# Kernel tuning notes

Measured on AMD Instinct MI355X. Metric: run time of the kernel, lower is better.

## Reference

```python
import jax, jax.numpy as jnp
import numpy as np


def setup_inputs() -> dict:
    key = jax.random.key(0)
    ks = jax.random.split(key, 7)
    b, c, h, w = 4, 256, 64, 64
    ci = c // 2
    inp = {
        "x0": jax.random.normal(ks[0], (b, 2 * c, h, w), dtype=jnp.float32),
        "x": jax.random.normal(ks[1], (b, c, h, w), dtype=jnp.float32),
        "x_dsm": jax.random.normal(ks[2], (b, c, h, w), dtype=jnp.float32),
        # 1x1 conv weights, stored as [out_ch, in_ch]
        "w_phi": jax.random.normal(ks[3], (ci, c), dtype=jnp.float32) * 0.02,
        "w_theta": jax.random.normal(ks[4], (ci, c), dtype=jnp.float32) * 0.02,
        "w_g": jax.random.normal(ks[5], (c, 2 * c), dtype=jnp.float32) * 0.02,
        "w_mask": jax.random.normal(ks[6], (2 * c, c), dtype=jnp.float32) * 0.02,
    }
    return inp


def reference(x0, x, x_dsm, w_phi, w_theta, w_g, w_mask):
    b, c, h, w = x.shape
    ci = c // 2
    n = h * w
    # 1x1 convs as channel matmuls
    phi = jnp.einsum('oc,bchw->bohw', w_phi, x).reshape(b, ci, n)            # [b, ci, N]
    theta = jnp.einsum('oc,bchw->bohw', w_theta, x_dsm).reshape(b, ci, n)    # [b, ci, N]
    theta = theta.transpose(0, 2, 1)                                         # [b, N, ci]
    g = jnp.einsum('oc,bchw->bohw', w_g, x0).reshape(b, c, n).transpose(0, 2, 1)  # [b, N, c]
    scores = jnp.matmul(theta, phi)                                          # [b, N, N]
    # NOTE: original uses nn.Softmax(dim=1) -> normalize over the FIRST N axis
    attn = jax.nn.softmax(scores, axis=1)
    out = jnp.matmul(attn, g)                                                # [b, N, c]
    out = out.transpose(0, 2, 1).reshape(b, c, h, w)
    mask = jnp.einsum('oc,bchw->bohw', w_mask, out)                          # [b, 2c, h, w]
    return mask + x0
```

## Files before the change

### kernel.cpp

```cpp
#include <hip/hip_runtime.h>
#include <math.h>

#define NB 4
#define NC 256
#define NCI 128
#define NC2 512
#define NPOS 4096
#define ISPLIT 8

using bf16x8 = __attribute__((ext_vector_type(8))) short;
using f32x4  = __attribute__((ext_vector_type(4))) float;
using f32x16 = __attribute__((ext_vector_type(16))) float;

__device__ inline unsigned short f2bf(float f) {
  unsigned int u = __float_as_uint(f);
  u = (u + 0x7fffu + ((u >> 16) & 1u)) >> 16;
  return (unsigned short)u;
}
__device__ inline float bf2f(short s) {
  return __uint_as_float(((unsigned int)(unsigned short)s) << 16);
}

__global__ void k_cast4(const float* __restrict__ s0, short* __restrict__ d0, int n0,
                        const float* __restrict__ s1, short* __restrict__ d1, int n1,
                        const float* __restrict__ s2, short* __restrict__ d2, int n2,
                        const float* __restrict__ s3, short* __restrict__ d3, int n3) {
  int i = blockIdx.x * 256 + threadIdx.x;
  if (i < n0) { d0[i] = (short)f2bf(s0[i]); return; } i -= n0;
  if (i < n1) { d1[i] = (short)f2bf(s1[i]); return; } i -= n1;
  if (i < n2) { d2[i] = (short)f2bf(s2[i]); return; } i -= n2;
  if (i < n3) { d3[i] = (short)f2bf(s3[i]); }
}

__global__ __launch_bounds__(256) void k_tcast_all(
    const float* __restrict__ x, const float* __restrict__ xdsm,
    const float* __restrict__ x0, short* __restrict__ xT,
    short* __restrict__ xdT, short* __restrict__ x0T) {
  __shared__ float t[64][65];
  const int tid = threadIdx.x;
  const int y = blockIdx.y, c0 = blockIdx.x * 64, b = blockIdx.z;
  const float* in; short* out; int R, r0;
  if (y < 4)      { in = x;    out = xT;  R = NC;  r0 = y * 64; }
  else if (y < 8) { in = xdsm; out = xdT; R = NC;  r0 = (y - 4) * 64; }
  else            { in = x0;   out = x0T; R = NC2; r0 = (y - 8) * 64; }
  const size_t inBs = (size_t)R * NPOS, outBs = (size_t)NPOS * R;
  {
    int r = tid >> 2, cc = (tid & 3) * 16;
    const float* ib = in + (size_t)b * inBs + (size_t)(r0 + r) * NPOS + c0 + cc;
#pragma unroll
    for (int i = 0; i < 4; ++i) {
      float4 v = *(const float4*)(ib + i * 4);
      t[r][cc + i * 4 + 0] = v.x; t[r][cc + i * 4 + 1] = v.y;
      t[r][cc + i * 4 + 2] = v.z; t[r][cc + i * 4 + 3] = v.w;
    }
  }
  __syncthreads();
  {
    int c = tid >> 2, rr = (tid & 3) * 16;
    __align__(16) short v[16];
#pragma unroll
    for (int i = 0; i < 16; ++i) v[i] = (short)f2bf(t[rr + i][c]);
    short* ob = out + (size_t)b * outBs + (size_t)(c0 + c) * R + r0 + rr;
    *(int4*)(ob) = *(const int4*)(v);
    *(int4*)(ob + 8) = *(const int4*)(v + 8);
  }
}

__global__ __launch_bounds__(256) void k_tcast4(
    const short* __restrict__ inP, short* __restrict__ out) {
  __shared__ float t[64][65];
  const int tid = threadIdx.x;
  const int r0 = blockIdx.y * 64, c0 = blockIdx.x * 64, b = blockIdx.z;
  {
    int r = tid >> 2, cc = (tid & 3) * 16;
    float tacc[16] = {};
#pragma unroll
    for (int p = 0; p < 4; ++p) {
      const short* ib = inP + ((size_t)p * NB + b) * NC * NPOS +
                        (size_t)(r0 + r) * NPOS + c0 + cc;
      bf16x8 a = *(const bf16x8*)(ib);
      bf16x8 a2 = *(const bf16x8*)(ib + 8);
#pragma unroll
      for (int i = 0; i < 8; ++i) { tacc[i] += bf2f(a[i]); tacc[8 + i] += bf2f(a2[i]); }
    }
#pragma unroll
    for (int i = 0; i < 16; ++i) t[r][cc + i] = tacc[i];
  }
  __syncthreads();
  {
    int c = tid >> 2, rr = (tid & 3) * 16;
    __align__(16) short v[16];
#pragma unroll
    for (int i = 0; i < 16; ++i) v[i] = (short)f2bf(t[rr + i][c]);
    short* ob = out + (size_t)b * (size_t)NPOS * NC + (size_t)(c0 + c) * NC + r0 + rr;
    *(int4*)(ob) = *(const int4*)(v);
    *(int4*)(ob + 8) = *(const int4*)(v + 8);
  }
}

template<bool OUT_BF16, bool HAS_RES>
__global__ __launch_bounds__(256, 2) void k_gemm(
    const short* __restrict__ A, const short* __restrict__ B,
    void* __restrict__ outv, const float* __restrict__ res,
    int K, int sN, size_t aBs, size_t bBs, size_t oBs) {
  __shared__ short As[2][64 * 64];
  __shared__ short Bs_[2][64 * 64];
  const int tid = threadIdx.x, lane = tid & 63, w = tid >> 6;
  const int x = lane & 15, q = lane >> 4;
  const int wm = (w & 1) * 32, wn = (w >> 1) * 32;
  const int n0 = blockIdx.x * 64, m0 = blockIdx.y * 64, b = blockIdx.z;
  const short* Ab = A + (size_t)b * aBs + (size_t)m0 * K;
  const short* Bb = B + (size_t)b * bBs + (size_t)n0 * K;
  const int r = tid >> 2, cth = tid & 3;
  f32x4 acc[2][2];
  acc[0][0] = acc[0][1] = acc[1][0] = acc[1][1] = (f32x4){0.f, 0.f, 0.f, 0.f};
  int4 ra[2], rb[2];
  const int NK = K >> 6;
#define GLOAD(kt)                                                              \
  { _Pragma("unroll") for (int i = 0; i < 2; ++i) {                            \
      ra[i] = *(const int4*)(Ab + (size_t)r * K + (kt) * 64 + (cth + i * 4) * 8); \
      rb[i] = *(const int4*)(Bb + (size_t)r * K + (kt) * 64 + (cth + i * 4) * 8); } }
#define GWRITE(buf)                                                            \
  { _Pragma("unroll") for (int i = 0; i < 2; ++i) {                            \
      *(int4*)(&As[buf][r * 64 + (((cth + i * 4) ^ (r & 7)) * 8)]) = ra[i];    \
      *(int4*)(&Bs_[buf][r * 64 + (((cth + i * 4) ^ (r & 7)) * 8)]) = rb[i]; } }
  GLOAD(0); GWRITE(0); __syncthreads();
  int cur = 0;
  for (int kt = 0; kt < NK; ++kt) {
    if (kt + 1 < NK) GLOAD(kt + 1);
    bf16x8 af[2][2], bfr[2][2];
#pragma unroll
    for (int ms = 0; ms < 2; ++ms) {
      int rowm = wm + ms * 16 + x;
#pragma unroll
      for (int ks = 0; ks < 2; ++ks)
        af[ms][ks] = *(const bf16x8*)(&As[cur][rowm * 64 + (((ks * 4 + q) ^ (rowm & 7)) * 8)]);
    }
#pragma unroll
    for (int ns = 0; ns < 2; ++ns) {
      int rown = wn + ns * 16 + x;
#pragma unroll
      for (int ks = 0; ks < 2; ++ks)
        bfr[ns][ks] = *(const bf16x8*)(&Bs_[cur][rown * 64 + (((ks * 4 + q) ^ (rown & 7)) * 8)]);
    }
#pragma unroll
    for (int ms = 0; ms < 2; ++ms)
#pragma unroll
      for (int ns = 0; ns < 2; ++ns)
#pragma unroll
        for (int ks = 0; ks < 2; ++ks)
          acc[ms][ns] = __builtin_amdgcn_mfma_f32_16x16x32_bf16(
              af[ms][ks], bfr[ns][ks], acc[ms][ns], 0, 0, 0);
    if (kt + 1 < NK) GWRITE(cur ^ 1);
    __syncthreads();
    cur ^= 1;
  }
#pragma unroll
  for (int ms = 0; ms < 2; ++ms)
#pragma unroll
    for (int ns = 0; ns < 2; ++ns) {
      int n = n0 + wn + ns * 16 + x;
      int m = m0 + wm + ms * 16 + q * 4;
      size_t off = (size_t)b * oBs + (size_t)n * sN + m;
      if (OUT_BF16) {
        __align__(8) short pv[4];
#pragma unroll
        for (int j = 0; j < 4; ++j) pv[j] = (short)f2bf(acc[ms][ns][j]);
        *(uint2*)((short*)outv + off) = *(const uint2*)pv;
      } else {
        float4 v = {acc[ms][ns][0], acc[ms][ns][1], acc[ms][ns][2], acc[ms][ns][3]};
        if (HAS_RES) {
          float4 rv = *(const float4*)(res + off);
          v.x += rv.x; v.y += rv.y; v.z += rv.z; v.w += rv.w;
        }
        *(float4*)((float*)outv + off) = v;
      }
    }
#undef GLOAD
#undef GWRITE
}

__global__ __launch_bounds__(256, 4) void k_lsum(
    const short* __restrict__ phiB, const short* __restrict__ thetaB,
    float* __restrict__ plsum) {
  __shared__ short thT[2][64 * 128];
  const int tid = threadIdx.x, lane = tid & 63, w = tid >> 6;
  const int x = lane & 15, q = lane >> 4;
  const int j0 = blockIdx.x * 64, iy = blockIdx.y, b = blockIdx.z;
  const short* phb = phiB + (size_t)b * NPOS * NCI;
  const short* thb = thetaB + (size_t)b * NPOS * NCI + (size_t)iy * (NPOS / ISPLIT) * NCI;
  bf16x8 af[4];
  {
    const short* pr = phb + (size_t)(j0 + w * 16 + x) * NCI;
#pragma unroll
    for (int kk = 0; kk < 4; ++kk) af[kk] = *(const bf16x8*)(pr + kk * 32 + q * 8);
  }
  float lsum[4] = {0.f, 0.f, 0.f, 0.f};
  int4 rt[4];
  const int NIT = NPOS / ISPLIT / 64;
#define LSUM_LOAD(it)                                                         \
  { _Pragma("unroll") for (int r = 0; r < 4; ++r) {                           \
      int s = tid + r * 256; int row = s >> 4, c = s & 15;                    \
      rt[r] = *(const int4*)(thb + (size_t)((it) * 64 + row) * NCI + c * 8); } }
#define LSUM_WRITE(buf)                                                       \
  { _Pragma("unroll") for (int r = 0; r < 4; ++r) {                           \
      int s = tid + r * 256; int row = s >> 4, c = s & 15;                    \
      *(int4*)(&thT[buf][row * 128 + ((c ^ (row & 7)) * 8)]) = rt[r]; } }
  LSUM_LOAD(0); LSUM_WRITE(0); __syncthreads();
  int cur = 0;
  for (int it = 0; it < NIT; ++it) {
    if (it + 1 < NIT) LSUM_LOAD(it + 1);
#pragma unroll
    for (int ii = 0; ii < 4; ++ii) {
      f32x4 s = {0.f, 0.f, 0.f, 0.f};
      int row = ii * 16 + x;
      int sw = row & 7;
#pragma unroll
      for (int kk = 0; kk < 4; ++kk) {
        bf16x8 bfv = *(const bf16x8*)(&thT[cur][row * 128 + (((kk * 4 + q) ^ sw) * 8)]);
        s = __builtin_amdgcn_mfma_f32_16x16x32_bf16(af[kk], bfv, s, 0, 0, 0);
      }
#pragma unroll
      for (int r = 0; r < 4; ++r) lsum[r] += __expf(s[r]);
    }
    if (it + 1 < NIT) LSUM_WRITE(cur ^ 1);
    __syncthreads();
    cur ^= 1;
  }
#pragma unroll
  for (int m = 1; m < 16; m <<= 1)
#pragma unroll
    for (int r = 0; r < 4; ++r) lsum[r] += __shfl_xor(lsum[r], m);
  if (x == 0) {
#pragma unroll
    for (int r = 0; r < 4; ++r)
      plsum[((size_t)(b * ISPLIT + iy) << 12) + j0 + w * 16 + 4 * q + r] = lsum[r];
  }
#undef LSUM_LOAD
#undef LSUM_WRITE
}

__global__ void k_lcomb(const float* __restrict__ plsum, float* __restrict__ linv) {
  int i = blockIdx.x * 256 + threadIdx.x;
  int b = i >> 12, j = i & (NPOS - 1);
  float s = 0.f;
#pragma unroll
  for (int t = 0; t < ISPLIT; ++t) s += plsum[((size_t)(b * ISPLIT + t) << 12) + j];
  linv[i] = 1.0f / s;
}

__global__ void k_scale_g(short* __restrict__ gB, const float* __restrict__ linv) {
  size_t e = ((size_t)blockIdx.x * 256 + threadIdx.x) * 8;
  int b = (int)(e >> 20);
  int p = (int)(e & (NPOS - 1));
  __align__(16) short v[8];
  *(int4*)v = *(const int4*)(gB + e);
  const float* lv = linv + ((size_t)b << 12) + p;
#pragma unroll
  for (int k = 0; k < 8; ++k) v[k] = (short)f2bf(bf2f(v[k]) * lv[k]);
  *(int4*)(gB + e) = *(const int4*)v;
}

__global__ __launch_bounds__(256, 2) void k_attn(
    const short* __restrict__ phiB, const short* __restrict__ thetaB,
    const short* __restrict__ gB, short* __restrict__ omidP) {
  __shared__ short phiT[2][32 * 128];
  __shared__ short gT[2][256 * 32];
  __shared__ short pT[4][32 * 32];
  const int tid = threadIdx.x, lane = tid & 63, w = tid >> 6;
  const int il = lane & 31, h = lane >> 5;
  const int key = (il >> 1) & 3;
  const int i0 = blockIdx.x * 128, jq = blockIdx.y, b = blockIdx.z;
  const short* phb = phiB + (size_t)b * NPOS * NCI;
  const short* thb = thetaB + (size_t)b * NPOS * NCI;
  const short* gb = gB + (size_t)b * NC * NPOS;
  short* om = omidP + ((size_t)(jq * NB + b)) * NC * NPOS;

  bf16x8 tf[8];
  {
    const short* tr = thb + (size_t)(i0 + w * 32 + il) * NCI;
#pragma unroll
    for (int kk = 0; kk < 8; ++kk) tf[kk] = *(const bf16x8*)(tr + kk * 16 + h * 8);
  }
  f32x16 acc[8];
#pragma unroll
  for (int i = 0; i < 8; ++i)
#pragma unroll
    for (int r = 0; r < 16; ++r) acc[i][r] = 0.f;

  int4 rphi[2], rg[4];
  const int NT = 32;
  const int jbase = jq * 32;
#define ATTN_LOAD(jt)                                                          \
  { _Pragma("unroll") for (int r = 0; r < 2; ++r) {                            \
      int s = tid + r * 256; int row = s >> 4, c = s & 15;                     \
      rphi[r] = *(const int4*)(phb + (size_t)((jbase + (jt)) * 32 + row) * NCI + c * 8); } \
    _Pragma("unroll") for (int r = 0; r < 4; ++r) {                            \
      int s = tid + r * 256; int cc = s >> 2, c4 = s & 3;                      \
      rg[r] = *(const int4*)(gb + (size_t)cc * NPOS + (jbase + (jt)) * 32 + c4 * 8); } }
#define ATTN_WRITE(buf)                                                        \
  { _Pragma("unroll") for (int r = 0; r < 2; ++r) {                            \
      int s = tid + r * 256; int row = s >> 4, c = s & 15;                     \
      *(int4*)(&phiT[buf][row * 128 + ((c ^ (row & 7)) * 8)]) = rphi[r]; }     \
    _Pragma("unroll") for (int r = 0; r < 4; ++r) {                            \
      int s = tid + r * 256; int cc = s >> 2, c4 = s & 3;                      \
      *(int4*)(&gT[buf][cc * 32 + ((c4 ^ ((cc >> 1) & 3)) * 8)]) = rg[r]; } }
  ATTN_LOAD(0); ATTN_WRITE(0); __syncthreads();
  int cur = 0;
  for (int jt = 0; jt < NT; ++jt) {
    if (jt + 1 < NT) ATTN_LOAD(jt + 1);
    {
      const short* PH = &phiT[cur][0];
      short* PW = &pT[w][0];
      f32x16 s16;
#pragma unroll
      for (int r = 0; r < 16; ++r) s16[r] = 0.f;
      const int swp = il & 7;
#pragma unroll
      for (int kk = 0; kk < 8; ++kk) {
        bf16x8 a = *(const bf16x8*)(PH + il * 128 + (((2 * kk + h) ^ swp) * 8));
        s16 = __builtin_amdgcn_mfma_f32_32x32x16_bf16(a, tf[kk], s16, 0, 0, 0);
      }
#pragma unroll
      for (int g2 = 0; g2 < 4; ++g2) {
        unsigned short p0 = f2bf(__expf(s16[4 * g2 + 0]));
        unsigned short p1 = f2bf(__expf(s16[4 * g2 + 1]));
        unsigned short p2 = f2bf(__expf(s16[4 * g2 + 2]));
        unsigned short p3 = f2bf(__expf(s16[4 * g2 + 3]));
        unsigned int lo = (unsigned int)p0 | ((unsigned int)p1 << 16);
        unsigned int hi2 = (unsigned int)p2 | ((unsigned int)p3 << 16);
        *(uint2*)(PW + il * 32 + ((g2 ^ key) * 8) + 4 * h) = make_uint2(lo, hi2);
      }
      const short* GT = &gT[cur][0];
      bf16x8 pa[2];
#pragma unroll
      for (int jh2 = 0; jh2 < 2; ++jh2)
        pa[jh2] = *(const bf16x8*)(PW + il * 32 + (((2 * jh2 + h) ^ key) * 8));
#pragma unroll
      for (int ct = 0; ct < 8; ++ct) {
#pragma unroll
        for (int jh2 = 0; jh2 < 2; ++jh2) {
          bf16x8 bg = *(const bf16x8*)(GT + (ct * 32 + il) * 32 + (((2 * jh2 + h) ^ key) * 8));
          acc[ct] = __builtin_amdgcn_mfma_f32_32x32x16_bf16(pa[jh2], bg, acc[ct], 0, 0, 0);
        }
      }
    }
    if (jt + 1 < NT) ATTN_WRITE(cur ^ 1);
    __syncthreads();
    cur ^= 1;
  }
#pragma unroll
  for (int ct = 0; ct < 8; ++ct)
#pragma unroll
    for (int g2 = 0; g2 < 4; ++g2) {
      __align__(8) short pv[4];
#pragma unroll
      for (int e = 0; e < 4; ++e) pv[e] = (short)f2bf(acc[ct][4 * g2 + e]);
      size_t o = (size_t)(ct * 32 + il) * NPOS + i0 + w * 32 + 8 * g2 + 4 * h;
      *(uint2*)(om + o) = *(const uint2*)pv;
    }
#undef ATTN_LOAD
#undef ATTN_WRITE
}

extern "C" void kernel_launch(void* const* d_in, const int* in_sizes, int n_in,
                              void* d_out, int out_size, void* d_ws, size_t ws_size,
                              hipStream_t stream) {
  (void)in_sizes; (void)n_in; (void)out_size; (void)ws_size;
  const float* x0      = (const float*)d_in[0];
  const float* x       = (const float*)d_in[1];
  const float* x_dsm   = (const float*)d_in[2];
  const float* w_phi   = (const float*)d_in[3];
  const float* w_theta = (const float*)d_in[4];
  const float* w_g     = (const float*)d_in[5];
  const float* w_mask  = (const float*)d_in[6];
  float* outp = (float*)d_out;

  short* sp = (short*)d_ws;
  short* wb_phi   = sp; sp += 32768;
  short* wb_theta = sp; sp += 32768;
  short* wb_g     = sp; sp += 131072;
  short* wb_mask  = sp; sp += 131072;
  short* xT   = sp; sp += (size_t)NB * NPOS * NC;
  short* xdT  = sp; sp += (size_t)NB * NPOS * NC;
  short* x0T  = sp; sp += (size_t)NB * NPOS * NC2;
  short* phiB   = sp; sp += (size_t)NB * NPOS * NCI;
  short* thetaB = sp; sp += (size_t)NB * NPOS * NCI;
  short* gBuf   = sp; sp += (size_t)NB * NC * NPOS;
  float* linv = (float*)sp; sp += 2 * (size_t)NB * NPOS;
  float* plsum = (float*)sp;
  short* omidP = xT;
  short* omidT = phiB;

  k_cast4<<<dim3(1280), 256, 0, stream>>>(w_phi, wb_phi, 32768,
                                          w_theta, wb_theta, 32768,
                                          w_g, wb_g, 131072,
                                          w_mask, wb_mask, 131072);

  k_tcast_all<<<dim3(64, 16, NB), 256, 0, stream>>>(x, x_dsm, x0, xT, xdT, x0T);

  k_gemm<true, false><<<dim3(64, 2, NB), 256, 0, stream>>>(
      wb_phi, xT, phiB, nullptr, NC, NCI, 0, (size_t)NPOS * NC, (size_t)NPOS * NCI);
  k_gemm<true, false><<<dim3(64, 2, NB), 256, 0, stream>>>(
      wb_theta, xdT, thetaB, nullptr, NC, NCI, 0, (size_t)NPOS * NC, (size_t)NPOS * NCI);
  k_gemm<true, false><<<dim3(4, 64, NB), 256, 0, stream>>>(
      x0T, wb_g, gBuf, nullptr, NC2, NPOS, (size_t)NPOS * NC2, 0, (size_t)NC * NPOS);

  k_lsum<<<dim3(NPOS / 64, ISPLIT, NB), 256, 0, stream>>>(phiB, thetaB, plsum);
  k_lcomb<<<dim3(NB * NPOS / 256), 256, 0, stream>>>(plsum, linv);
  k_scale_g<<<dim3(2048), 256, 0, stream>>>(gBuf, linv);

  k_attn<<<dim3(NPOS / 128, 4, NB), 256, 0, stream>>>(phiB, thetaB, gBuf, omidP);

  k_tcast4<<<dim3(64, 4, NB), 256, 0, stream>>>(omidP, omidT);

  k_gemm<false, true><<<dim3(8, 64, NB), 256, 0, stream>>>(
      omidT, wb_mask, outp, x0, NC, NPOS, (size_t)NPOS * NC, 0, (size_t)NC2 * NPOS);
}
```

Measured before the change: 236.9 us.

## Rewrite column-sum kernel with 32x32x16 MFMA and 128-column blocks

The softmax denominator kernel now computes each tile with 32x32x16 bf16 MFMAs, so every wave covers 32 phi columns instead of 16 and each block covers 128 columns. The theta tile per iteration shrinks to 32 rows, and theta is placed in the A operand so the 16 accumulator values per lane all belong to one output column. That lets the per-lane exp sums be combined with a single cross-half shuffle instead of a 16-lane butterfly. The intent is to halve the grid and the redundant theta LDS traffic per column and to reduce per-tile overhead. In exchange it needs more registers for the phi fragments and runs twice as many, shorter loop iterations, with more barriers.

```diff
diff --git a/kernel.cpp b/kernel.cpp
--- a/kernel.cpp
+++ b/kernel.cpp
@@ -183,59 +183,51 @@
 __global__ __launch_bounds__(256, 4) void k_lsum(
     const short* __restrict__ phiB, const short* __restrict__ thetaB,
     float* __restrict__ plsum) {
-  __shared__ short thT[2][64 * 128];
+  __shared__ short thT[2][32 * 128];
   const int tid = threadIdx.x, lane = tid & 63, w = tid >> 6;
-  const int x = lane & 15, q = lane >> 4;
-  const int j0 = blockIdx.x * 64, iy = blockIdx.y, b = blockIdx.z;
+  const int il = lane & 31, h = lane >> 5;
+  const int j0 = blockIdx.x * 128, iy = blockIdx.y, b = blockIdx.z;
   const short* phb = phiB + (size_t)b * NPOS * NCI;
   const short* thb = thetaB + (size_t)b * NPOS * NCI + (size_t)iy * (NPOS / ISPLIT) * NCI;
-  bf16x8 af[4];
-  {
-    const short* pr = phb + (size_t)(j0 + w * 16 + x) * NCI;
-#pragma unroll
-    for (int kk = 0; kk < 4; ++kk) af[kk] = *(const bf16x8*)(pr + kk * 32 + q * 8);
-  }
-  float lsum[4] = {0.f, 0.f, 0.f, 0.f};
-  int4 rt[4];
-  const int NIT = NPOS / ISPLIT / 64;
+  bf16x8 pf[8];
+  {
+    const short* pr = phb + (size_t)(j0 + w * 32 + il) * NCI;
+#pragma unroll
+    for (int kk = 0; kk < 8; ++kk) pf[kk] = *(const bf16x8*)(pr + kk * 16 + h * 8);
+  }
+  float lsum = 0.f;
+  int4 rt[2];
+  const int NIT = NPOS / ISPLIT / 32;
 #define LSUM_LOAD(it)                                                         \
-  { _Pragma("unroll") for (int r = 0; r < 4; ++r) {                           \
+  { _Pragma("unroll") for (int r = 0; r < 2; ++r) {                           \
       int s = tid + r * 256; int row = s >> 4, c = s & 15;                    \
-      rt[r] = *(const int4*)(thb + (size_t)((it) * 64 + row) * NCI + c * 8); } }
+      rt[r] = *(const int4*)(thb + (size_t)((it) * 32 + row) * NCI + c * 8); } }
 #define LSUM_WRITE(buf)                                                       \
-  { _Pragma("unroll") for (int r = 0; r < 4; ++r) {                           \
+  { _Pragma("unroll") for (int r = 0; r < 2; ++r) {                           \
       int s = tid + r * 256; int row = s >> 4, c = s & 15;                    \
       *(int4*)(&thT[buf][row * 128 + ((c ^ (row & 7)) * 8)]) = rt[r]; } }
   LSUM_LOAD(0); LSUM_WRITE(0); __syncthreads();
   int cur = 0;
+  const int swz = il & 7;
   for (int it = 0; it < NIT; ++it) {
     if (it + 1 < NIT) LSUM_LOAD(it + 1);
-#pragma unroll
-    for (int ii = 0; ii < 4; ++ii) {
-      f32x4 s = {0.f, 0.f, 0.f, 0.f};
-      int row = ii * 16 + x;
-      int sw = row & 7;
-#pragma unroll
-      for (int kk = 0; kk < 4; ++kk) {
-        bf16x8 bfv = *(const bf16x8*)(&thT[cur][row * 128 + (((kk * 4 + q) ^ sw) * 8)]);
-        s = __builtin_amdgcn_mfma_f32_16x16x32_bf16(af[kk], bfv, s, 0, 0, 0);
-      }
-#pragma unroll
-      for (int r = 0; r < 4; ++r) lsum[r] += __expf(s[r]);
-    }
+    f32x16 s16;
+#pragma unroll
+    for (int r = 0; r < 16; ++r) s16[r] = 0.f;
+#pragma unroll
+    for (int kk = 0; kk < 8; ++kk) {
+      bf16x8 a = *(const bf16x8*)(&thT[cur][il * 128 + (((2 * kk + h) ^ swz) * 8)]);
+      s16 = __builtin_amdgcn_mfma_f32_32x32x16_bf16(a, pf[kk], s16, 0, 0, 0);
+    }
+#pragma unroll
+    for (int r = 0; r < 16; ++r) lsum += __expf(s16[r]);
     if (it + 1 < NIT) LSUM_WRITE(cur ^ 1);
     __syncthreads();
     cur ^= 1;
   }
-#pragma unroll
-  for (int m = 1; m < 16; m <<= 1)
-#pragma unroll
-    for (int r = 0; r < 4; ++r) lsum[r] += __shfl_xor(lsum[r], m);
-  if (x == 0) {
-#pragma unroll
-    for (int r = 0; r < 4; ++r)
-      plsum[((size_t)(b * ISPLIT + iy) << 12) + j0 + w * 16 + 4 * q + r] = lsum[r];
-  }
+  lsum += __shfl_xor(lsum, 32);
+  if (h == 0)
+    plsum[((size_t)(b * ISPLIT + iy) << 12) + j0 + w * 32 + il] = lsum;
 #undef LSUM_LOAD
 #undef LSUM_WRITE
 }
@@ -406,7 +398,7 @@
   k_gemm<true, false><<<dim3(4, 64, NB), 256, 0, stream>>>(
       x0T, wb_g, gBuf, nullptr, NC2, NPOS, (size_t)NPOS * NC2, 0, (size_t)NC * NPOS);
 
-  k_lsum<<<dim3(NPOS / 64, ISPLIT, NB), 256, 0, stream>>>(phiB, thetaB, plsum);
+  k_lsum<<<dim3(NPOS / 128, ISPLIT, NB), 256, 0, stream>>>(phiB, thetaB, plsum);
   k_lcomb<<<dim3(NB * NPOS / 256), 256, 0, stream>>>(plsum, linv);
   k_scale_g<<<dim3(2048), 256, 0, stream>>>(gBuf, linv);
 
```

Measured after the change: 231.7 us. 1.02x faster.
